# Kernel optimization log

Measured on AMD Instinct MI355X. Metric: run time of the kernel, lower is better.

The kernel has to match this reference:

```python
import jax, jax.numpy as jnp
import numpy as np

N, E, B, V, ED, M = 100000, 1600000, 100, 10000, 16, 64
EPS = 1e-5

def _seg_mean(x, ids, n):
    s = jax.ops.segment_sum(x, ids, num_segments=n)
    c = jax.ops.segment_sum(jnp.ones((x.shape[0], 1), x.dtype), ids, num_segments=n)
    return s / jnp.maximum(c, 1.0)

def _graph_conv(x, src, dst, ew, w_rel, b_rel, w_root):
    # PyG GraphConv: out = lin_rel(sum_j e_ji * x_j) + lin_root(x)
    msg = x[src] * ew[:, None]                       # [E, din] gather + weight
    agg = jax.ops.segment_sum(msg, dst, num_segments=x.shape[0])  # scatter-add
    return agg @ w_rel + b_rel + x @ w_root

def _graph_norm(x, batch, g, b, a):
    m = _seg_mean(x, batch, B)
    xc = x - a * m[batch]
    v = _seg_mean(xc * xc, batch, B)
    return g * xc / jnp.sqrt(v[batch] + EPS) + b

def _lrelu(x):
    return jnp.where(x > 0, x, 0.01 * x)

def _bn(x, g, b):
    m = x.mean(0)
    v = x.var(0)
    return g * (x - m) / jnp.sqrt(v + EPS) + b

def setup_inputs() -> dict:
    key = jax.random.key(0)
    ks = jax.random.split(key, 36)
    def lin(k, din, dout):
        return jax.random.normal(k, (din, dout), jnp.float32) / np.sqrt(din)
    d = {
        'x_idx': jax.random.randint(ks[0], (N,), 0, V),
        'edge_index': jax.random.randint(ks[1], (2, E), 0, N),
        'edge_attr': jax.random.uniform(ks[2], (E, 1), jnp.float32),
        'batch': jnp.sort(jax.random.randint(ks[3], (N,), 0, B)),
        'demographics': jax.random.normal(ks[4], (B, 4), jnp.float32),
        'emb': jax.random.normal(ks[5], (V, ED), jnp.float32),
        'w_rel1': lin(ks[6], ED, M),   'b_rel1': jnp.zeros((M,), jnp.float32),   'w_root1': lin(ks[7], ED, M),
        'w_rel2': lin(ks[8], M, 2*M),  'b_rel2': jnp.zeros((2*M,), jnp.float32), 'w_root2': lin(ks[9], M, 2*M),
        'w_rel3': lin(ks[10], 2*M, 4*M),'b_rel3': jnp.zeros((4*M,), jnp.float32),'w_root3': lin(ks[11], 2*M, 4*M),
        'gn1_g': jnp.ones((M,), jnp.float32),   'gn1_b': jnp.zeros((M,), jnp.float32),   'gn1_a': jnp.ones((M,), jnp.float32),
        'gn2_g': jnp.ones((2*M,), jnp.float32), 'gn2_b': jnp.zeros((2*M,), jnp.float32), 'gn2_a': jnp.ones((2*M,), jnp.float32),
        'demo_w': lin(ks[12], 4, 16), 'demo_b': jnp.zeros((16,), jnp.float32),
        'l1_w': lin(ks[13], 4*M + 16, 2*M), 'l1_b': jnp.zeros((2*M,), jnp.float32),
        'bn1_g': jnp.ones((2*M,), jnp.float32), 'bn1_b': jnp.zeros((2*M,), jnp.float32),
        'l2_w': lin(ks[14], 2*M, M), 'l2_b': jnp.zeros((M,), jnp.float32),
        'bn2_g': jnp.ones((M,), jnp.float32), 'bn2_b': jnp.zeros((M,), jnp.float32),
        'l3_w': lin(ks[15], M, 3), 'l3_b': jnp.zeros((3,), jnp.float32),
    }
    return d

def reference(x_idx, edge_index, edge_attr, batch, demographics, emb,
              w_rel1, b_rel1, w_root1, w_rel2, b_rel2, w_root2, w_rel3, b_rel3, w_root3,
              gn1_g, gn1_b, gn1_a, gn2_g, gn2_b, gn2_a,
              demo_w, demo_b, l1_w, l1_b, bn1_g, bn1_b, l2_w, l2_b, bn2_g, bn2_b, l3_w, l3_b):
    src, dst = edge_index[0], edge_index[1]
    ew = edge_attr[:, 0]                  # squeeze(-1)
    x = emb[x_idx]                        # [N, 16]
    x = _graph_conv(x, src, dst, ew, w_rel1, b_rel1, w_root1)
    x = _lrelu(_graph_norm(x, batch, gn1_g, gn1_b, gn1_a))
    x = _graph_conv(x, src, dst, ew, w_rel2, b_rel2, w_root2)
    x = _lrelu(_graph_norm(x, batch, gn2_g, gn2_b, gn2_a))
    x = _graph_conv(x, src, dst, ew, w_rel3, b_rel3, w_root3)   # [N, 256]
    gf = _seg_mean(x, batch, B)                                  # global_mean_pool [B, 256]
    demo = demographics @ demo_w + demo_b                        # [B, 16]
    h = jnp.concatenate([gf, demo], axis=1)                      # [B, 272]
    h = _lrelu(_bn(h @ l1_w + l1_b, bn1_g, bn1_b))               # dropout = identity (eval)
    h = _lrelu(_bn(h @ l2_w + l2_b, bn2_g, bn2_b))
    return h @ l3_w + l3_b                                       # [B, 3]
```

## Files before the change

kernel.cpp:

```cpp
#include <hip/hip_runtime.h>

#define NN 100000
#define NE 1600000
#define NBATCH 100
#define NBUCK 391
constexpr float EPS = 1e-5f;

typedef unsigned short ushort_t;
typedef unsigned int uint_t;
typedef unsigned char uchar_t;

using short8 = __attribute__((ext_vector_type(8))) short;
using floatx4 = __attribute__((ext_vector_type(4))) float;
using floatx2 = __attribute__((ext_vector_type(2))) float;

__device__ __forceinline__ float lrelu(float x) { return x > 0.f ? x : 0.01f * x; }

__device__ __forceinline__ float b2f(ushort_t u) {
    union { uint_t i; float f; } c; c.i = ((uint_t)u) << 16; return c.f;
}
__device__ __forceinline__ ushort_t f2b(float f) {
    union { float f; uint_t i; } c; c.f = f;
    uint_t u = c.i;
    return (ushort_t)((u + 0x7FFFu + ((u >> 16) & 1u)) >> 16);
}
__device__ __forceinline__ void unpack8(const uint4 u, float* f) {
    f[0] = b2f(u.x & 0xffff); f[1] = b2f(u.x >> 16);
    f[2] = b2f(u.y & 0xffff); f[3] = b2f(u.y >> 16);
    f[4] = b2f(u.z & 0xffff); f[5] = b2f(u.z >> 16);
    f[6] = b2f(u.w & 0xffff); f[7] = b2f(u.w >> 16);
}
__device__ __forceinline__ void unpack8_f8(const uint2 u, float* f) {
    floatx2 a = __builtin_amdgcn_cvt_pk_f32_fp8(u.x, false);
    floatx2 b = __builtin_amdgcn_cvt_pk_f32_fp8(u.x, true);
    floatx2 c = __builtin_amdgcn_cvt_pk_f32_fp8(u.y, false);
    floatx2 d = __builtin_amdgcn_cvt_pk_f32_fp8(u.y, true);
    f[0] = a[0]; f[1] = a[1]; f[2] = b[0]; f[3] = b[1];
    f[4] = c[0]; f[5] = c[1]; f[6] = d[0]; f[7] = d[1];
}


__global__ __launch_bounds__(256) void k_bcount(const int* __restrict__ dst,
                                                int* __restrict__ bcnt) {
    __shared__ int h[NBUCK];
    for (int i = threadIdx.x; i < NBUCK; i += 256) h[i] = 0;
    __syncthreads();
    for (int e = blockIdx.x * 256 + threadIdx.x; e < NE; e += gridDim.x * 256)
        atomicAdd(&h[dst[e] >> 8], 1);
    __syncthreads();
    for (int i = threadIdx.x; i < NBUCK; i += 256)
        if (h[i]) atomicAdd(&bcnt[i], h[i]);
}

__global__ __launch_bounds__(512) void k_bscan(const int* __restrict__ bcnt,
                                               int* __restrict__ bbase,
                                               int* __restrict__ bcur,
                                               int* __restrict__ rowstart) {
    __shared__ int s[512];
    const int t = threadIdx.x;
    const int v = (t < NBUCK) ? bcnt[t] : 0;
    s[t] = v;
    __syncthreads();
    for (int off = 1; off < 512; off <<= 1) {
        int o = (t >= off) ? s[t - off] : 0;
        __syncthreads();
        s[t] += o;
        __syncthreads();
    }
    const int excl = s[t] - v;
    if (t < NBUCK) { bbase[t] = excl; bcur[t] = excl; }
    if (t == 0) { bbase[NBUCK] = NE; rowstart[NN] = NE; }
}

__global__ __launch_bounds__(256) void k_bscatter(const int* __restrict__ dst,
                                                  const int* __restrict__ srcv,
                                                  const float* __restrict__ ew,
                                                  int* __restrict__ bcur,
                                                  int2* __restrict__ ebuf) {
    __shared__ int h[NBUCK];
    __shared__ int lcur[NBUCK];
    const int chunk = (NE + gridDim.x - 1) / gridDim.x;
    const int beg = blockIdx.x * chunk;
    const int end = (beg + chunk < NE) ? beg + chunk : NE;
    for (int i = threadIdx.x; i < NBUCK; i += 256) h[i] = 0;
    __syncthreads();
    for (int e = beg + threadIdx.x; e < end; e += 256)
        atomicAdd(&h[dst[e] >> 8], 1);
    __syncthreads();
    for (int i = threadIdx.x; i < NBUCK; i += 256)
        lcur[i] = h[i] ? atomicAdd(&bcur[i], h[i]) : 0;
    __syncthreads();
    for (int e = beg + threadIdx.x; e < end; e += 256) {
        const int d = dst[e];
        const int pos = atomicAdd(&lcur[d >> 8], 1);
        ebuf[pos] = make_int2(srcv[e] | ((d & 255) << 20), __float_as_int(ew[e]));
    }
}

__global__ __launch_bounds__(256) void k_bfinal(const int2* __restrict__ ebuf,
                                                const int* __restrict__ bbase,
                                                int* __restrict__ rowstart,
                                                int2* __restrict__ csr_pair) {
    __shared__ int h[256];
    __shared__ int cur[256];
    const int b = blockIdx.x;
    const int t = threadIdx.x;
    const int base = bbase[b];
    const int cnt = bbase[b + 1] - base;
    h[t] = 0;
    __syncthreads();
    for (int i = t; i < cnt; i += 256)
        atomicAdd(&h[(ebuf[base + i].x >> 20) & 255], 1);
    __syncthreads();
    const int v = h[t];
    cur[t] = v;
    __syncthreads();
    for (int off = 1; off < 256; off <<= 1) {
        int o = (t >= off) ? cur[t - off] : 0;
        __syncthreads();
        cur[t] += o;
        __syncthreads();
    }
    const int excl = cur[t] - v;
    const int n = (b << 8) + t;
    if (n < NN) rowstart[n] = base + excl;
    __syncthreads();
    cur[t] = excl;
    __syncthreads();
    for (int i = t; i < cnt; i += 256) {
        const int2 p = ebuf[base + i];
        const int loc = (p.x >> 20) & 255;
        const int pos = base + atomicAdd(&cur[loc], 1);
        csr_pair[pos] = make_int2(p.x & 0xFFFFF, p.y);
    }
}

__global__ void k_bounds(const int* __restrict__ batch, int* __restrict__ bstart) {
    int b = blockIdx.x * blockDim.x + threadIdx.x;
    if (b > NBATCH) return;
    int lo = 0, hi = NN;
    while (lo < hi) {
        int mid = (lo + hi) >> 1;
        if (batch[mid] < b) lo = mid + 1; else hi = mid;
    }
    bstart[b] = lo;
}


__global__ void k_wpack(const float* __restrict__ wr1, const float* __restrict__ wo1,
                        const float* __restrict__ wr2, const float* __restrict__ wo2,
                        const float* __restrict__ wr3, const float* __restrict__ wo3,
                        ushort_t* __restrict__ w1T, ushort_t* __restrict__ w2T,
                        ushort_t* __restrict__ w3T) {
    int idx = blockIdx.x * blockDim.x + threadIdx.x;
    if (idx < 2048) {
        int n = idx >> 5, k = idx & 31;
        float v = (k < 16) ? wr1[k * 64 + n] : wo1[(k - 16) * 64 + n];
        w1T[idx] = f2b(v);
    } else if (idx < 2048 + 16384) {
        int l = idx - 2048; int n = l >> 7, k = l & 127;
        float v = (k < 64) ? wr2[k * 128 + n] : wo2[(k - 64) * 128 + n];
        w2T[l] = f2b(v);
    } else if (idx < 2048 + 16384 + 65536) {
        int l = idx - 18432; int n = l >> 8, k = l & 255;
        float v = (k < 128) ? wr3[k * 256 + n] : wo3[(k - 128) * 256 + n];
        w3T[l] = f2b(v);
    }
}


__global__ void k_gather_b(const int* __restrict__ xi, const float* __restrict__ emb,
                           ushort_t* __restrict__ xcat0) {
    int n = blockIdx.x * blockDim.x + threadIdx.x;
    if (n >= NN) return;
    const float* e = emb + ((size_t)xi[n] << 4);
    uint_t u[8];
#pragma unroll
    for (int j = 0; j < 8; ++j)
        u[j] = (uint_t)f2b(e[2 * j]) | ((uint_t)f2b(e[2 * j + 1]) << 16);
    uint4* o = (uint4*)(xcat0 + (size_t)n * 32 + 16);
    o[0] = {u[0], u[1], u[2], u[3]};
    o[1] = {u[4], u[5], u[6], u[7]};
}


template <int D>
__global__ void k_aggregate_b(ushort_t* __restrict__ xcat, const int2* __restrict__ csr_pair,
                              const int* __restrict__ rowstart) {
    constexpr int LPN = D / 8;
    constexpr int EP = 64 / LPN;
    const int n = blockIdx.x * 4 + (threadIdx.x >> 6);
    const int lane = threadIdx.x & 63;
    const int sl = lane % LPN;
    const int eg = lane / LPN;
    if (n >= NN) return;
    const int beg = rowstart[n], end = rowstart[n + 1];
    float a0[8] = {}, a1[8] = {};
    int i = beg + eg;
    for (; i + EP < end; i += 2 * EP) {
        const int2 p0 = csr_pair[i];
        const int2 p1 = csr_pair[i + EP];
        const float w0 = __int_as_float(p0.y);
        const float w1 = __int_as_float(p1.y);
        const uint4 u0 = *(const uint4*)(xcat + (size_t)p0.x * (2 * D) + D + sl * 8);
        const uint4 u1 = *(const uint4*)(xcat + (size_t)p1.x * (2 * D) + D + sl * 8);
        float f0[8], f1[8];
        unpack8(u0, f0); unpack8(u1, f1);
#pragma unroll
        for (int j = 0; j < 8; ++j) { a0[j] += f0[j] * w0; a1[j] += f1[j] * w1; }
    }
    if (i < end) {
        const int2 p0 = csr_pair[i];
        const float w0 = __int_as_float(p0.y);
        const uint4 u0 = *(const uint4*)(xcat + (size_t)p0.x * (2 * D) + D + sl * 8);
        float f0[8];
        unpack8(u0, f0);
#pragma unroll
        for (int j = 0; j < 8; ++j) a0[j] += f0[j] * w0;
    }
#pragma unroll
    for (int j = 0; j < 8; ++j) a0[j] += a1[j];
#pragma unroll
    for (int m = LPN; m < 64; m <<= 1)
#pragma unroll
        for (int j = 0; j < 8; ++j) a0[j] += __shfl_xor(a0[j], m);
    if (eg == 0) {
        uint_t u[4];
#pragma unroll
        for (int j = 0; j < 4; ++j)
            u[j] = (uint_t)f2b(a0[2 * j]) | ((uint_t)f2b(a0[2 * j + 1]) << 16);
        *(uint4*)(xcat + (size_t)n * (2 * D) + sl * 8) = {u[0], u[1], u[2], u[3]};
    }
}


__global__ void k_aggregate_f8(ushort_t* __restrict__ xcat, const uchar_t* __restrict__ x8,
                               const int2* __restrict__ csr_pair, const int* __restrict__ rowstart) {
    constexpr int D = 128;
    constexpr int LPN = 16;
    constexpr int EP = 4;
    const int n = blockIdx.x * 4 + (threadIdx.x >> 6);
    const int lane = threadIdx.x & 63;
    const int sl = lane % LPN;
    const int eg = lane / LPN;
    if (n >= NN) return;
    const int beg = rowstart[n], end = rowstart[n + 1];
    float a0[8] = {}, a1[8] = {};
    int i = beg + eg;
    for (; i + EP < end; i += 2 * EP) {
        const int2 p0 = csr_pair[i];
        const int2 p1 = csr_pair[i + EP];
        const float w0 = __int_as_float(p0.y);
        const float w1 = __int_as_float(p1.y);
        const uint2 u0 = *(const uint2*)(x8 + (size_t)p0.x * D + sl * 8);
        const uint2 u1 = *(const uint2*)(x8 + (size_t)p1.x * D + sl * 8);
        float f0[8], f1[8];
        unpack8_f8(u0, f0); unpack8_f8(u1, f1);
#pragma unroll
        for (int j = 0; j < 8; ++j) { a0[j] += f0[j] * w0; a1[j] += f1[j] * w1; }
    }
    if (i < end) {
        const int2 p0 = csr_pair[i];
        const float w0 = __int_as_float(p0.y);
        const uint2 u0 = *(const uint2*)(x8 + (size_t)p0.x * D + sl * 8);
        float f0[8];
        unpack8_f8(u0, f0);
#pragma unroll
        for (int j = 0; j < 8; ++j) a0[j] += f0[j] * w0;
    }
#pragma unroll
    for (int j = 0; j < 8; ++j) a0[j] += a1[j];
#pragma unroll
    for (int m = LPN; m < 64; m <<= 1)
#pragma unroll
        for (int j = 0; j < 8; ++j) a0[j] += __shfl_xor(a0[j], m);
    if (eg == 0) {
        uint_t u[4];
#pragma unroll
        for (int j = 0; j < 4; ++j)
            u[j] = (uint_t)f2b(a0[2 * j]) | ((uint_t)f2b(a0[2 * j + 1]) << 16);
        *(uint4*)(xcat + (size_t)n * (2 * D) + sl * 8) = {u[0], u[1], u[2], u[3]};
    }
}


template <int K2, int DOUT, int MODE>
__global__ __launch_bounds__(256) void k_conv_mfma(
        const ushort_t* __restrict__ xcat, const ushort_t* __restrict__ wcatT,
        const float* __restrict__ brel, float* __restrict__ outp,
        const int* __restrict__ batch, const int* __restrict__ bstart,
        float* __restrict__ sacc, float* __restrict__ qacc) {
    constexpr int CW = DOUT / 64;
    const int lane = threadIdx.x & 63;
    const int wv = threadIdx.x >> 6;
    const int m = lane & 15;
    const int quad = lane >> 4;
    const int r0 = blockIdx.x * 64;

    floatx4 acc[4][CW] = {};

    const ushort_t* arow[4];
#pragma unroll
    for (int r = 0; r < 4; ++r) {
        int an = r0 + r * 16 + m; if (an >= NN) an = NN - 1;
        arow[r] = xcat + (size_t)an * K2 + quad * 8;
    }
    const ushort_t* brow[CW];
#pragma unroll
    for (int c = 0; c < CW; ++c)
        brow[c] = wcatT + (size_t)((wv * CW + c) * 16 + m) * K2 + quad * 8;

    for (int kk = 0; kk < K2; kk += 32) {
        short8 a[4], b[CW];
#pragma unroll
        for (int r = 0; r < 4; ++r) a[r] = *(const short8*)(arow[r] + kk);
#pragma unroll
        for (int c = 0; c < CW; ++c) b[c] = *(const short8*)(brow[c] + kk);
#pragma unroll
        for (int r = 0; r < 4; ++r)
#pragma unroll
            for (int c = 0; c < CW; ++c)
                acc[r][c] = __builtin_amdgcn_mfma_f32_16x16x32_bf16(a[r], b[c], acc[r][c], 0, 0, 0);
    }

    float bias[CW];
#pragma unroll
    for (int c = 0; c < CW; ++c) bias[c] = brel[(wv * CW + c) * 16 + m];

    if constexpr (MODE == 1) {
#pragma unroll
        for (int c = 0; c < CW; ++c) {
            const int col = (wv * CW + c) * 16 + m;
#pragma unroll
            for (int r = 0; r < 4; ++r)
#pragma unroll
                for (int rr = 0; rr < 4; ++rr) {
                    const int row = r0 + r * 16 + quad * 4 + rr;
                    if (row < NN)
                        outp[(size_t)row * DOUT + col] = acc[r][c][rr] + bias[c];
                }
        }
        const int rtop = (r0 + 63 < NN) ? r0 + 63 : NN - 1;
        const int sb0 = batch[r0];
        const int sb1 = batch[rtop];
        for (int sb = sb0; sb <= sb1; ++sb) {
            const int lo = (bstart[sb] > r0) ? bstart[sb] : r0;
            int hi = bstart[sb + 1];
            if (hi > r0 + 64) hi = r0 + 64;
            float s[CW], q[CW];
#pragma unroll
            for (int c = 0; c < CW; ++c) { s[c] = 0.f; q[c] = 0.f; }
#pragma unroll
            for (int r = 0; r < 4; ++r)
#pragma unroll
                for (int rr = 0; rr < 4; ++rr) {
                    const int row = r0 + r * 16 + quad * 4 + rr;
                    if (row >= lo && row < hi) {
#pragma unroll
                        for (int c = 0; c < CW; ++c) {
                            const float v = acc[r][c][rr] + bias[c];
                            s[c] += v; q[c] += v * v;
                        }
                    }
                }
#pragma unroll
            for (int c = 0; c < CW; ++c) {
                s[c] += __shfl_xor(s[c], 16); s[c] += __shfl_xor(s[c], 32);
                q[c] += __shfl_xor(q[c], 16); q[c] += __shfl_xor(q[c], 32);
            }
            if (quad == 0) {
#pragma unroll
                for (int c = 0; c < CW; ++c) {
                    const int col = (wv * CW + c) * 16 + m;
                    atomicAdd(&sacc[sb * DOUT + col], s[c]);
                    atomicAdd(&qacc[sb * DOUT + col], q[c]);
                }
            }
        }
    } else {
        const int rtop = (r0 + 63 < NN) ? r0 + 63 : NN - 1;
        const int sb0 = batch[r0];
        const int sb1 = batch[rtop];
        for (int sb = sb0; sb <= sb1; ++sb) {
            const int lo = (bstart[sb] > r0) ? bstart[sb] : r0;
            int hi = bstart[sb + 1];
            if (hi > r0 + 64) hi = r0 + 64;
            float s[CW];
#pragma unroll
            for (int c = 0; c < CW; ++c) s[c] = 0.f;
#pragma unroll
            for (int r = 0; r < 4; ++r)
#pragma unroll
                for (int rr = 0; rr < 4; ++rr) {
                    const int row = r0 + r * 16 + quad * 4 + rr;
                    if (row >= lo && row < hi) {
#pragma unroll
                        for (int c = 0; c < CW; ++c) s[c] += acc[r][c][rr] + bias[c];
                    }
                }
#pragma unroll
            for (int c = 0; c < CW; ++c) {
                s[c] += __shfl_xor(s[c], 16);
                s[c] += __shfl_xor(s[c], 32);
            }
            if (quad == 0) {
#pragma unroll
                for (int c = 0; c < CW; ++c)
                    atomicAdd(&sacc[sb * 256 + (wv * CW + c) * 16 + m], s[c]);
            }
        }
    }
}

__global__ void k_gffin(const float* __restrict__ gfacc, const int* __restrict__ bstart,
                        float* __restrict__ h0) {
    int idx = blockIdx.x * blockDim.x + threadIdx.x;
    if (idx >= NBATCH * 256) return;
    int b = idx >> 8, c = idx & 255;
    float cnt = fmaxf((float)(bstart[b + 1] - bstart[b]), 1.f);
    h0[b * 272 + c] = gfacc[idx] / cnt;
}


template <int D, int OST, bool F8>
__global__ __launch_bounds__(256) void k_gnapply(
        const float* __restrict__ xf, ushort_t* __restrict__ xout, uchar_t* __restrict__ x8out,
        const int* __restrict__ bstart, const float* __restrict__ sacc,
        const float* __restrict__ qacc, const float* __restrict__ a,
        const float* __restrict__ g, const float* __restrict__ bb) {
    const int b = blockIdx.x;
    const int col0 = blockIdx.y * 64;
    const int c4 = (threadIdx.x & 15) * 4;
    const int rg = threadIdx.x >> 4;
    const int beg = bstart[b], end = bstart[b + 1];
    const float cntf = fmaxf((float)(end - beg), 1.f);

    const float4 S = *(const float4*)&sacc[b * D + col0 + c4];
    const float4 Q = *(const float4*)&qacc[b * D + col0 + c4];
    const float4 al4 = *(const float4*)&a[col0 + c4];
    const float4 g4 = *(const float4*)&g[col0 + c4];
    const float4 bb4 = *(const float4*)&bb[col0 + c4];
    float mean[4], inv[4];
    const float Sv[4] = {S.x, S.y, S.z, S.w};
    const float Qv[4] = {Q.x, Q.y, Q.z, Q.w};
    const float av[4] = {al4.x, al4.y, al4.z, al4.w};
#pragma unroll
    for (int c = 0; c < 4; ++c) {
        const float mm = Sv[c] / cntf;
        const float ex2 = Qv[c] / cntf;
        const float var = fmaxf(ex2 - mm * mm * (2.f * av[c] - av[c] * av[c]), 0.f);
        mean[c] = mm;
        inv[c] = 1.f / sqrtf(var + EPS);
    }
    for (int r = beg + rg; r < end; r += 16) {
        const float4 v = *(const float4*)&xf[(size_t)r * D + col0 + c4];
        const float y0 = lrelu(g4.x * (v.x - av[0] * mean[0]) * inv[0] + bb4.x);
        const float y1 = lrelu(g4.y * (v.y - av[1] * mean[1]) * inv[1] + bb4.y);
        const float y2 = lrelu(g4.z * (v.z - av[2] * mean[2]) * inv[2] + bb4.z);
        const float y3 = lrelu(g4.w * (v.w - av[3] * mean[3]) * inv[3] + bb4.w);
        uint2 o;
        o.x = (uint_t)f2b(y0) | ((uint_t)f2b(y1) << 16);
        o.y = (uint_t)f2b(y2) | ((uint_t)f2b(y3) << 16);
        *(uint2*)&xout[(size_t)r * OST + col0 + c4] = o;
        if constexpr (F8) {
            uint_t p = __builtin_amdgcn_cvt_pk_fp8_f32(y0, y1, 0, false);
            p = __builtin_amdgcn_cvt_pk_fp8_f32(y2, y3, p, true);
            *(uint_t*)&x8out[(size_t)r * D + col0 + c4] = p;
        }
    }
}

__global__ void k_demo(const float* __restrict__ dg, const float* __restrict__ w,
                       const float* __restrict__ b, float* __restrict__ h0) {
    int idx = blockIdx.x * blockDim.x + threadIdx.x;
    if (idx < NBATCH * 16) {
        int i = idx >> 4, j = idx & 15;
        float acc = b[j];
        for (int k = 0; k < 4; ++k) acc += dg[i * 4 + k] * w[k * 16 + j];
        h0[i * 272 + 256 + j] = acc;
    }
}


template <int K, int C>
__global__ __launch_bounds__(C) void k_head_lin(const float* __restrict__ in,
                                                const float* __restrict__ w,
                                                const float* __restrict__ bias,
                                                float* __restrict__ z, int rows) {
    __shared__ float s_in[16][K];
    const int j = threadIdx.x;
    const int r0 = blockIdx.x * 16;
    for (int idx = threadIdx.x; idx < 16 * K; idx += C) {
        int r = idx / K, k = idx - r * K;
        s_in[r][k] = (r0 + r < rows) ? in[(size_t)(r0 + r) * K + k] : 0.f;
    }
    __syncthreads();
    float acc[16];
#pragma unroll
    for (int r = 0; r < 16; ++r) acc[r] = 0.f;
    for (int k = 0; k < K; ++k) {
        const float wv = w[k * C + j];
#pragma unroll
        for (int r = 0; r < 16; ++r) acc[r] += s_in[r][k] * wv;
    }
    const float bj = bias[j];
#pragma unroll
    for (int r = 0; r < 16; ++r)
        if (r0 + r < rows) z[(size_t)(r0 + r) * C + j] = acc[r] + bj;
}

__global__ void k_head_bn(float* __restrict__ z, const float* __restrict__ g,
                          const float* __restrict__ b, int rows, int C) {
    const int j = threadIdx.x;
    if (j >= C) return;
    float s = 0.f, q = 0.f;
    for (int i = 0; i < rows; ++i) { const float v = z[i * C + j]; s += v; q += v * v; }
    const float m = s / rows;
    const float var = fmaxf(q / rows - m * m, 0.f);
    const float inv = 1.f / sqrtf(var + EPS);
    const float gg = g[j], bb = b[j];
    for (int i = 0; i < rows; ++i)
        z[i * C + j] = lrelu(gg * (z[i * C + j] - m) * inv + bb);
}

__global__ __launch_bounds__(256) void k_head_out(const float* __restrict__ h2,
                                                  const float* __restrict__ w,
                                                  const float* __restrict__ b,
                                                  float* __restrict__ out) {
    __shared__ float s[NBATCH * 65];
    for (int idx = threadIdx.x; idx < NBATCH * 64; idx += 256) {
        int i = idx >> 6, k = idx & 63;
        s[i * 65 + k] = h2[idx];
    }
    __syncthreads();
    const int i = threadIdx.x;
    if (i < NBATCH) {
        float a0 = b[0], a1 = b[1], a2 = b[2];
        for (int k = 0; k < 64; ++k) {
            const float v = s[i * 65 + k];
            a0 += v * w[k * 3 + 0];
            a1 += v * w[k * 3 + 1];
            a2 += v * w[k * 3 + 2];
        }
        out[i * 3 + 0] = a0; out[i * 3 + 1] = a1; out[i * 3 + 2] = a2;
    }
}


extern "C" void kernel_launch(void* const* d_in, const int* in_sizes, int n_in,
                              void* d_out, int out_size, void* d_ws, size_t ws_size,
                              hipStream_t stream) {
    const int*   x_idx  = (const int*)d_in[0];
    const int*   ei     = (const int*)d_in[1];
    const float* eattr  = (const float*)d_in[2];
    const int*   batch  = (const int*)d_in[3];
    const float* demog  = (const float*)d_in[4];
    const float* emb    = (const float*)d_in[5];
    const float* wrel1  = (const float*)d_in[6];
    const float* brel1  = (const float*)d_in[7];
    const float* wroot1 = (const float*)d_in[8];
    const float* wrel2  = (const float*)d_in[9];
    const float* brel2  = (const float*)d_in[10];
    const float* wroot2 = (const float*)d_in[11];
    const float* wrel3  = (const float*)d_in[12];
    const float* brel3  = (const float*)d_in[13];
    const float* wroot3 = (const float*)d_in[14];
    const float* gn1g = (const float*)d_in[15];
    const float* gn1b = (const float*)d_in[16];
    const float* gn1a = (const float*)d_in[17];
    const float* gn2g = (const float*)d_in[18];
    const float* gn2b = (const float*)d_in[19];
    const float* gn2a = (const float*)d_in[20];
    const float* dw   = (const float*)d_in[21];
    const float* db   = (const float*)d_in[22];
    const float* l1w  = (const float*)d_in[23];
    const float* l1b  = (const float*)d_in[24];
    const float* bn1g = (const float*)d_in[25];
    const float* bn1b = (const float*)d_in[26];
    const float* l2w  = (const float*)d_in[27];
    const float* l2b  = (const float*)d_in[28];
    const float* bn2g = (const float*)d_in[29];
    const float* bn2b = (const float*)d_in[30];
    const float* l3w  = (const float*)d_in[31];
    const float* l3b  = (const float*)d_in[32];
    float* out = (float*)d_out;

    float*    W     = (float*)d_ws;
    float*    xf    = W;
    int2*     ebuf  = (int2*)W;
    float*    gfacc = W + 12800000;
    ushort_t* xcat0 = (ushort_t*)(W + 25600000);
    ushort_t* xcat1 = (ushort_t*)(W + 27200000);
    ushort_t* xcat2 = (ushort_t*)(W + 33600000);
    ushort_t* w1T   = (ushort_t*)(W + 46400000);
    ushort_t* w2T   = w1T + 2048;
    ushort_t* w3T   = w2T + 16384;
    int2*     csr_pair = (int2*)(W + 46450000);
    int*      rowstart = (int*)(W + 49650000);
    int*      bstart   = (int*)(W + 49760000);
    int*      bcnt     = (int*)(W + 49761000);
    int*      bbase    = (int*)(W + 49762000);
    int*      bcur     = (int*)(W + 49763000);
    float*    h0 = W + 49770000;
    float*    h1 = h0 + 27200;
    float*    h2 = h1 + 12800;
    float*    sacc1 = W + 49817000;
    float*    qacc1 = sacc1 + 6400;
    float*    sacc2 = W + 49830000;
    float*    qacc2 = sacc2 + 12800;
    uchar_t*  x8    = (uchar_t*)(W + 49860000);

    const int* src = ei;
    const int* dst = ei + NE;

    const int mfma_blk = (NN + 63) / 64;
    const int nagg_blk = (NN + 3) / 4;

    hipMemsetAsync(bcnt, 0, NBUCK * sizeof(int), stream);
    k_bcount<<<256, 256, 0, stream>>>(dst, bcnt);
    k_bscan<<<1, 512, 0, stream>>>(bcnt, bbase, bcur, rowstart);
    k_bscatter<<<256, 256, 0, stream>>>(dst, src, eattr, bcur, ebuf);
    k_bfinal<<<NBUCK, 256, 0, stream>>>(ebuf, bbase, rowstart, csr_pair);

    k_bounds<<<1, 128, 0, stream>>>(batch, bstart);
    k_wpack<<<(83968 + 255) / 256, 256, 0, stream>>>(wrel1, wroot1, wrel2, wroot2, wrel3, wroot3,
                                                     w1T, w2T, w3T);
    hipMemsetAsync(gfacc, 0, NBATCH * 256 * sizeof(float), stream);
    hipMemsetAsync(sacc1, 0, (6400 * 2) * sizeof(float), stream);
    hipMemsetAsync(sacc2, 0, (12800 * 2) * sizeof(float), stream);

    k_gather_b<<<(NN + 255) / 256, 256, 0, stream>>>(x_idx, emb, xcat0);

    k_aggregate_b<16><<<nagg_blk, 256, 0, stream>>>(xcat0, csr_pair, rowstart);
    k_conv_mfma<32, 64, 1><<<mfma_blk, 256, 0, stream>>>(xcat0, w1T, brel1, xf, batch, bstart, sacc1, qacc1);
    k_gnapply<64, 128, false><<<dim3(NBATCH, 1), 256, 0, stream>>>(xf, xcat1 + 64, nullptr,
                                                                   bstart, sacc1, qacc1, gn1a, gn1g, gn1b);

    k_aggregate_b<64><<<nagg_blk, 256, 0, stream>>>(xcat1, csr_pair, rowstart);
    k_conv_mfma<128, 128, 1><<<mfma_blk, 256, 0, stream>>>(xcat1, w2T, brel2, xf, batch, bstart, sacc2, qacc2);
    k_gnapply<128, 256, true><<<dim3(NBATCH, 2), 256, 0, stream>>>(xf, xcat2 + 128, x8,
                                                                   bstart, sacc2, qacc2, gn2a, gn2g, gn2b);

    k_aggregate_f8<<<nagg_blk, 256, 0, stream>>>(xcat2, x8, csr_pair, rowstart);
    k_conv_mfma<256, 256, 2><<<mfma_blk, 256, 0, stream>>>(xcat2, w3T, brel3, nullptr, batch, bstart, gfacc, nullptr);

    k_gffin<<<(NBATCH * 256 + 255) / 256, 256, 0, stream>>>(gfacc, bstart, h0);
    k_demo<<<(NBATCH * 16 + 255) / 256, 256, 0, stream>>>(demog, dw, db, h0);
    k_head_lin<272, 128><<<(NBATCH + 15) / 16, 128, 0, stream>>>(h0, l1w, l1b, h1, NBATCH);
    k_head_bn<<<1, 128, 0, stream>>>(h1, bn1g, bn1b, NBATCH, 128);
    k_head_lin<128, 64><<<(NBATCH + 15) / 16, 64, 0, stream>>>(h1, l2w, l2b, h2, NBATCH);
    k_head_bn<<<1, 64, 0, stream>>>(h2, bn2g, bn2b, NBATCH, 64);
    k_head_out<<<1, 256, 0, stream>>>(h2, l3w, l3b, out);
}
```

Measured before the change: 650.2 us.

## Pre-swizzle weights into MFMA fragment order and split-K the third conv

Weight packing now writes the bf16 weights directly in per-lane MFMA fragment order, so every B-operand load becomes one contiguous 16-byte read per lane instead of a strided row access. The K loop is fully unrolled. The layer-3 conv is split along K across two grid slices that both accumulate into the pooled sums, which is valid because MODE 2 only does linear atomic pooling and the bias is added only by slice 0. This doubles the block count for the largest GEMM at the cost of more atomic traffic and three packing launches instead of one.

```diff
diff --git a/kernel.cpp b/kernel.cpp
--- a/kernel.cpp
+++ b/kernel.cpp
@@ -147,25 +147,17 @@
 }
 
 
-__global__ void k_wpack(const float* __restrict__ wr1, const float* __restrict__ wo1,
-                        const float* __restrict__ wr2, const float* __restrict__ wo2,
-                        const float* __restrict__ wr3, const float* __restrict__ wo3,
-                        ushort_t* __restrict__ w1T, ushort_t* __restrict__ w2T,
-                        ushort_t* __restrict__ w3T) {
-    int idx = blockIdx.x * blockDim.x + threadIdx.x;
-    if (idx < 2048) {
-        int n = idx >> 5, k = idx & 31;
-        float v = (k < 16) ? wr1[k * 64 + n] : wo1[(k - 16) * 64 + n];
-        w1T[idx] = f2b(v);
-    } else if (idx < 2048 + 16384) {
-        int l = idx - 2048; int n = l >> 7, k = l & 127;
-        float v = (k < 64) ? wr2[k * 128 + n] : wo2[(k - 64) * 128 + n];
-        w2T[l] = f2b(v);
-    } else if (idx < 2048 + 16384 + 65536) {
-        int l = idx - 18432; int n = l >> 8, k = l & 255;
-        float v = (k < 128) ? wr3[k * 256 + n] : wo3[(k - 128) * 256 + n];
-        w3T[l] = f2b(v);
-    }
+template <int K, int K2, int DOUT>
+__global__ void k_wpackf(const float* __restrict__ wrel, const float* __restrict__ wroot,
+                         ushort_t* __restrict__ wf) {
+    int idx = blockIdx.x * 256 + threadIdx.x;
+    if (idx >= DOUT * K2) return;
+    const int col = idx / K2, k = idx - col * K2;
+    const float v = (k < K) ? wrel[k * DOUT + col] : wroot[(k - K) * DOUT + col];
+    const int ct = col >> 4, m = col & 15;
+    const int kb = k >> 5, q = (k >> 3) & 3, j = k & 7;
+    const int lane = m + (q << 4);
+    wf[(((size_t)(ct * (K2 / 32) + kb) * 64 + lane) << 3) + j] = f2b(v);
 }
 
 
@@ -284,18 +276,21 @@
 }
 
 
-template <int K2, int DOUT, int MODE>
+template <int K2, int DOUT, int MODE, int NSPLIT>
 __global__ __launch_bounds__(256) void k_conv_mfma(
-        const ushort_t* __restrict__ xcat, const ushort_t* __restrict__ wcatT,
+        const ushort_t* __restrict__ xcat, const ushort_t* __restrict__ wfrag,
         const float* __restrict__ brel, float* __restrict__ outp,
         const int* __restrict__ batch, const int* __restrict__ bstart,
         float* __restrict__ sacc, float* __restrict__ qacc) {
     constexpr int CW = DOUT / 64;
+    constexpr int KBTOT = K2 / 32;
+    constexpr int KSTEPS = KBTOT / NSPLIT;
     const int lane = threadIdx.x & 63;
     const int wv = threadIdx.x >> 6;
     const int m = lane & 15;
     const int quad = lane >> 4;
     const int r0 = blockIdx.x * 64;
+    const int kb0 = blockIdx.y * KSTEPS;
 
     floatx4 acc[4][CW] = {};
 
@@ -303,19 +298,20 @@
 #pragma unroll
     for (int r = 0; r < 4; ++r) {
         int an = r0 + r * 16 + m; if (an >= NN) an = NN - 1;
-        arow[r] = xcat + (size_t)an * K2 + quad * 8;
-    }
-    const ushort_t* brow[CW];
+        arow[r] = xcat + (size_t)an * K2 + quad * 8 + kb0 * 32;
+    }
+    const ushort_t* bfr[CW];
 #pragma unroll
     for (int c = 0; c < CW; ++c)
-        brow[c] = wcatT + (size_t)((wv * CW + c) * 16 + m) * K2 + quad * 8;
-
-    for (int kk = 0; kk < K2; kk += 32) {
+        bfr[c] = wfrag + (((size_t)((wv * CW + c) * KBTOT + kb0) * 64 + lane) << 3);
+
+#pragma unroll
+    for (int s = 0; s < KSTEPS; ++s) {
         short8 a[4], b[CW];
 #pragma unroll
-        for (int r = 0; r < 4; ++r) a[r] = *(const short8*)(arow[r] + kk);
-#pragma unroll
-        for (int c = 0; c < CW; ++c) b[c] = *(const short8*)(brow[c] + kk);
+        for (int r = 0; r < 4; ++r) a[r] = *(const short8*)(arow[r] + s * 32);
+#pragma unroll
+        for (int c = 0; c < CW; ++c) b[c] = *(const short8*)(bfr[c] + (size_t)s * 512);
 #pragma unroll
         for (int r = 0; r < 4; ++r)
 #pragma unroll
@@ -325,7 +321,8 @@
 
     float bias[CW];
 #pragma unroll
-    for (int c = 0; c < CW; ++c) bias[c] = brel[(wv * CW + c) * 16 + m];
+    for (int c = 0; c < CW; ++c)
+        bias[c] = (NSPLIT == 1 || blockIdx.y == 0) ? brel[(wv * CW + c) * 16 + m] : 0.f;
 
     if constexpr (MODE == 1) {
 #pragma unroll
@@ -623,8 +620,9 @@
     k_bfinal<<<NBUCK, 256, 0, stream>>>(ebuf, bbase, rowstart, csr_pair);
 
     k_bounds<<<1, 128, 0, stream>>>(batch, bstart);
-    k_wpack<<<(83968 + 255) / 256, 256, 0, stream>>>(wrel1, wroot1, wrel2, wroot2, wrel3, wroot3,
-                                                     w1T, w2T, w3T);
+    k_wpackf<16, 32, 64><<<(2048 + 255) / 256, 256, 0, stream>>>(wrel1, wroot1, w1T);
+    k_wpackf<64, 128, 128><<<(16384 + 255) / 256, 256, 0, stream>>>(wrel2, wroot2, w2T);
+    k_wpackf<128, 256, 256><<<(65536 + 255) / 256, 256, 0, stream>>>(wrel3, wroot3, w3T);
     hipMemsetAsync(gfacc, 0, NBATCH * 256 * sizeof(float), stream);
     hipMemsetAsync(sacc1, 0, (6400 * 2) * sizeof(float), stream);
     hipMemsetAsync(sacc2, 0, (12800 * 2) * sizeof(float), stream);
@@ -632,17 +630,17 @@
     k_gather_b<<<(NN + 255) / 256, 256, 0, stream>>>(x_idx, emb, xcat0);
 
     k_aggregate_b<16><<<nagg_blk, 256, 0, stream>>>(xcat0, csr_pair, rowstart);
-    k_conv_mfma<32, 64, 1><<<mfma_blk, 256, 0, stream>>>(xcat0, w1T, brel1, xf, batch, bstart, sacc1, qacc1);
+    k_conv_mfma<32, 64, 1, 1><<<mfma_blk, 256, 0, stream>>>(xcat0, w1T, brel1, xf, batch, bstart, sacc1, qacc1);
     k_gnapply<64, 128, false><<<dim3(NBATCH, 1), 256, 0, stream>>>(xf, xcat1 + 64, nullptr,
                                                                    bstart, sacc1, qacc1, gn1a, gn1g, gn1b);
 
     k_aggregate_b<64><<<nagg_blk, 256, 0, stream>>>(xcat1, csr_pair, rowstart);
-    k_conv_mfma<128, 128, 1><<<mfma_blk, 256, 0, stream>>>(xcat1, w2T, brel2, xf, batch, bstart, sacc2, qacc2);
+    k_conv_mfma<128, 128, 1, 1><<<mfma_blk, 256, 0, stream>>>(xcat1, w2T, brel2, xf, batch, bstart, sacc2, qacc2);
     k_gnapply<128, 256, true><<<dim3(NBATCH, 2), 256, 0, stream>>>(xf, xcat2 + 128, x8,
                                                                    bstart, sacc2, qacc2, gn2a, gn2g, gn2b);
 
     k_aggregate_f8<<<nagg_blk, 256, 0, stream>>>(xcat2, x8, csr_pair, rowstart);
-    k_conv_mfma<256, 256, 2><<<mfma_blk, 256, 0, stream>>>(xcat2, w3T, brel3, nullptr, batch, bstart, gfacc, nullptr);
+    k_conv_mfma<256, 256, 2, 2><<<dim3(mfma_blk, 2), 256, 0, stream>>>(xcat2, w3T, brel3, nullptr, batch, bstart, gfacc, nullptr);
 
     k_gffin<<<(NBATCH * 256 + 255) / 256, 256, 0, stream>>>(gfacc, bstart, h0);
     k_demo<<<(NBATCH * 16 + 255) / 256, 256, 0, stream>>>(demog, dw, db, h0);
```

Measured after the change: 624.5 us. 4.0% less time.
